# Optimization experiments

Measured on AMD Instinct MI355X. Metric: run time of the kernel, lower is better.

Reference implementation:

```python
import jax, jax.numpy as jnp
import numpy as np

# static config (matches init_kwargs)
C, NH, WS, H, W, NQ, PS = 384, 12, 8, 56, 56, 64, 8
HD = C // NH
SCALE = HD ** -0.5
EPS = 1e-5
MLP_H = 4 * C


def _rel_pos_index():
    ch, cw = np.meshgrid(np.arange(WS), np.arange(WS), indexing='ij')
    cf = np.stack([ch.ravel(), cw.ravel()])                      # [2, WS*WS]
    rel = cf[:, :, None] - cf[:, None, :]                        # [2, N, N]
    rel = rel.transpose(1, 2, 0)
    rel[:, :, 0] += WS - 1
    rel[:, :, 1] += WS - 1
    rel[:, :, 0] *= 2 * WS - 1
    return jnp.asarray(rel.sum(-1))                              # [N, N] int

REL_IDX = _rel_pos_index()


def _ln(x, g, b):
    mu = x.mean(-1, keepdims=True)
    var = ((x - mu) ** 2).mean(-1, keepdims=True)
    return (x - mu) * jax.lax.rsqrt(var + EPS) * g + b


def setup_inputs() -> dict:
    key = jax.random.key(0)
    ks = jax.random.split(key, 24)
    B = 16
    n = lambda k, shp, s=0.02: jax.random.normal(k, shp, dtype=jnp.float32) * s
    inp = {
        'x': jax.random.normal(ks[0], (B, H * W, C), dtype=jnp.float32),
        'query_tokens': n(ks[1], (1, NQ, C)),
        'kproj_w': n(ks[2], (C, C)), 'kproj_b': jnp.zeros((C,)),
        'kbn_g': jnp.ones((C,)), 'kbn_b': jnp.zeros((C,)),
        'vproj_w': n(ks[3], (C, C)), 'vproj_b': jnp.zeros((C,)),
        'vbn_g': jnp.ones((C,)), 'vbn_b': jnp.zeros((C,)),
        'ck_w': n(ks[4], (C, C)), 'ck_b': jnp.zeros((C,)),
        'cv_w': n(ks[5], (C, C)), 'cv_b': jnp.zeros((C,)),
        'qkv_w': n(ks[6], (C, 3 * C)), 'qkv_b': jnp.zeros((3 * C,)),
        'proj_w': n(ks[7], (C, C)), 'proj_b': jnp.zeros((C,)),
        'rpb_table': n(ks[8], ((2 * WS - 1) ** 2, NH)),
        'norm1_g': jnp.ones((C,)), 'norm1_b': jnp.zeros((C,)),
        'norm2_g': jnp.ones((C,)), 'norm2_b': jnp.zeros((C,)),
        'fc1_w': n(ks[9], (C, MLP_H)), 'fc1_b': jnp.zeros((MLP_H,)),
        'fc2_w': n(ks[10], (MLP_H, C)), 'fc2_b': jnp.zeros((C,)),
    }
    return inp


def _forward(x, query_tokens, kproj_w, kproj_b, kbn_g, kbn_b, vproj_w, vproj_b,
             vbn_g, vbn_b, ck_w, ck_b, cv_w, cv_b, qkv_w, qkv_b, proj_w, proj_b,
             rpb_table, norm1_g, norm1_b, norm2_g, norm2_b, fc1_w, fc1_b, fc2_w, fc2_b):
    B, L, _ = x.shape
    shortcut = x
    xn = _ln(x, norm1_g, norm1_b)                                # [B, L, C]

    # ---- global cross attention (pooled tokens -> learnable queries) ----
    x4 = xn.reshape(B, H, W, C)
    pooled = x4.reshape(B, H // PS, PS, W // PS, PS, C).mean(axis=(2, 4))  # [B,7,7,C]
    pooled = pooled.reshape(B, (H // PS) * (W // PS), C)         # [B, 49, C]
    # conv1x1 + BatchNorm2d (eval mode, default running stats mean=0, var=1)
    bn_scale = 1.0 / jnp.sqrt(1.0 + EPS)
    key = ((pooled @ kproj_w + kproj_b) * bn_scale) * kbn_g + kbn_b
    val = ((pooled @ vproj_w + vproj_b) * bn_scale) * vbn_g + vbn_b

    q = jnp.broadcast_to(query_tokens, (B, NQ, C))
    qh = q.reshape(B, NQ, NH, HD).transpose(0, 2, 1, 3)          # [B,NH,NQ,HD]
    kh = key.reshape(B, -1, NH, HD).transpose(0, 2, 1, 3)
    vh = val.reshape(B, -1, NH, HD).transpose(0, 2, 1, 3)
    attn = jax.nn.softmax(jnp.einsum('bhqd,bhkd->bhqk', qh, kh) * SCALE, axis=-1)
    o = jnp.einsum('bhqk,bhkd->bhqd', attn, vh).transpose(0, 2, 1, 3).reshape(B, NQ, C)
    gk = (o + q) @ ck_w + ck_b                                   # [B, NQ, C]
    gv = (o + q) @ cv_w + cv_b

    # ---- windowed attention with global kv concat ----
    nW = (H // WS) * (W // WS)
    N = WS * WS
    xw = (x4.reshape(B, H // WS, WS, W // WS, WS, C)
             .transpose(0, 1, 3, 2, 4, 5)
             .reshape(B * nW, N, C))                             # [B_, N, C]
    qkv = (xw @ qkv_w + qkv_b).reshape(B * nW, N, 3, NH, HD).transpose(2, 0, 3, 1, 4)
    wq, wk, wv = qkv[0], qkv[1], qkv[2]                          # [B_, NH, N, HD]

    gkh = jnp.broadcast_to(gk.reshape(B, 1, NQ, NH, HD), (B, nW, NQ, NH, HD))
    gkh = gkh.reshape(B * nW, NQ, NH, HD).transpose(0, 2, 1, 3)  # [B_, NH, NQ, HD]
    gvh = jnp.broadcast_to(gv.reshape(B, 1, NQ, NH, HD), (B, nW, NQ, NH, HD))
    gvh = gvh.reshape(B * nW, NQ, NH, HD).transpose(0, 2, 1, 3)
    wk = jnp.concatenate([wk, gkh], axis=2)                      # [B_, NH, N+NQ, HD]
    wv = jnp.concatenate([wv, gvh], axis=2)

    logits = jnp.einsum('bhqd,bhkd->bhqk', wq * SCALE, wk)       # [B_, NH, N, N+NQ]
    rpb = rpb_table[REL_IDX.reshape(-1)].reshape(N, N, NH).transpose(2, 0, 1)  # [NH,N,N]
    logits = logits.at[:, :, :, :N].add(rpb[None])
    wattn = jax.nn.softmax(logits, axis=-1)
    ow = jnp.einsum('bhqk,bhkd->bhqd', wattn, wv).transpose(0, 2, 1, 3).reshape(B * nW, N, C)
    ow = ow @ proj_w + proj_b

    # window reverse
    xr = (ow.reshape(B, H // WS, W // WS, WS, WS, C)
             .transpose(0, 1, 3, 2, 4, 5)
             .reshape(B, H * W, C))

    x = shortcut + xr
    h = jax.nn.gelu(_ln(x, norm2_g, norm2_b) @ fc1_w + fc1_b, approximate=False)
    return x + (h @ fc2_w + fc2_b)


def reference(x, query_tokens, kproj_w, kproj_b, kbn_g, kbn_b, vproj_w, vproj_b,
              vbn_g, vbn_b, ck_w, ck_b, cv_w, cv_b, qkv_w, qkv_b, proj_w, proj_b,
              rpb_table, norm1_g, norm1_b, norm2_g, norm2_b, fc1_w, fc1_b, fc2_w, fc2_b):
    return _forward(x, query_tokens, kproj_w, kproj_b, kbn_g, kbn_b, vproj_w, vproj_b,
                    vbn_g, vbn_b, ck_w, ck_b, cv_w, cv_b, qkv_w, qkv_b, proj_w, proj_b,
                    rpb_table, norm1_g, norm1_b, norm2_g, norm2_b, fc1_w, fc1_b, fc2_w, fc2_b)
```

## Files before the change

kernel.cpp:

```cpp
#include <hip/hip_runtime.h>
#include <math.h>

typedef __attribute__((ext_vector_type(8))) __bf16 bf16x8;
typedef __attribute__((ext_vector_type(4))) float f32x4;
typedef __attribute__((ext_vector_type(8))) unsigned short u16x8;

#define DI __device__ __forceinline__

DI float b2f(unsigned short u) { return __uint_as_float(((unsigned int)u) << 16); }
DI unsigned short f2b(float f) {
    unsigned int x = __float_as_uint(f);
    x += 0x7fffu + ((x >> 16) & 1u);
    return (unsigned short)(x >> 16);
}
DI unsigned short f2b_fast(float f) {
    __bf16 h = (__bf16)f;
    return *(unsigned short*)&h;
}

DI void gl16(const unsigned short* g, unsigned short* l) {
    __builtin_amdgcn_global_load_lds(
        (const __attribute__((address_space(1))) void*)g,
        (__attribute__((address_space(3))) void*)l,
        16, 0, 0);
}

DI float gelu_f(float v) {
    float y = -1.5957691216f * v - 0.0713548163f * v * v * v;
    return v * __builtin_amdgcn_rcpf(1.f + __expf(y));
}

#define SCALE_ATT 0.17677669529663687f
#define BN_SCALE  0.9999950000374997f

__global__ __launch_bounds__(256) void cvt_t_kernel(const float* __restrict__ in,
                                                    unsigned short* __restrict__ out,
                                                    int Kd, int Nd) {
    int i = blockIdx.x * 256 + threadIdx.x;
    if (i < Kd * Nd) {
        int k = i / Nd, n = i % Nd;
        out[(size_t)n * Kd + k] = f2b(in[i]);
    }
}

__global__ __launch_bounds__(64) void ln_kernel(const float* __restrict__ xin,
                                                const float* __restrict__ g,
                                                const float* __restrict__ bsh,
                                                unsigned short* __restrict__ out) {
    int row = blockIdx.x;
    int t = threadIdx.x;
    size_t base = (size_t)row * 384;
    float v[6];
    float s = 0.f;
#pragma unroll
    for (int p = 0; p < 6; ++p) { v[p] = xin[base + t + 64 * p]; s += v[p]; }
#pragma unroll
    for (int off = 32; off > 0; off >>= 1) s += __shfl_xor(s, off);
    float mu = s * (1.f / 384.f);
    float q = 0.f;
#pragma unroll
    for (int p = 0; p < 6; ++p) { float d = v[p] - mu; q += d * d; }
#pragma unroll
    for (int off = 32; off > 0; off >>= 1) q += __shfl_xor(q, off);
    float rstd = rsqrtf(q * (1.f / 384.f) + 1e-5f);
#pragma unroll
    for (int p = 0; p < 6; ++p) {
        int c = t + 64 * p;
        out[base + c] = f2b((v[p] - mu) * rstd * g[c] + bsh[c]);
    }
}

__global__ __launch_bounds__(384) void pool_kernel(const unsigned short* __restrict__ xn,
                                                   float* __restrict__ pooled) {
    int blk = blockIdx.x;
    int b = blk / 49, pp = blk % 49;
    int ph = pp / 7, pw = pp % 7;
    int c = threadIdx.x;
    float s = 0.f;
    for (int i = 0; i < 8; ++i) {
        size_t rb = ((size_t)b * 3136 + (size_t)(ph * 8 + i) * 56 + pw * 8) * 384;
        for (int j = 0; j < 8; ++j) s += b2f(xn[rb + (size_t)j * 384 + c]);
    }
    pooled[(size_t)blk * 384 + c] = s * (1.f / 64.f);
}

__global__ __launch_bounds__(128) void kvproj_kernel(
    const float* __restrict__ pooled,
    const float* __restrict__ kw, const float* __restrict__ kb,
    const float* __restrict__ kg, const float* __restrict__ kbb,
    const float* __restrict__ vw, const float* __restrict__ vb,
    const float* __restrict__ vg, const float* __restrict__ vbb,
    float* __restrict__ keyo, float* __restrict__ valo) {
    __shared__ float row[384];
    int r = blockIdx.x;
    int t = threadIdx.x;
    for (int c = t; c < 384; c += 128) row[c] = pooled[(size_t)r * 384 + c];
    __syncthreads();
#pragma unroll
    for (int p = 0; p < 3; ++p) {
        int c = t + 128 * p;
        float aK = 0.f, aV = 0.f;
        for (int k = 0; k < 384; ++k) {
            float rv = row[k];
            aK += rv * kw[(size_t)k * 384 + c];
            aV += rv * vw[(size_t)k * 384 + c];
        }
        keyo[(size_t)r * 384 + c] = (aK + kb[c]) * BN_SCALE * kg[c] + kbb[c];
        valo[(size_t)r * 384 + c] = (aV + vb[c]) * BN_SCALE * vg[c] + vbb[c];
    }
}

__global__ __launch_bounds__(64) void rpb_expand_kernel(const float* __restrict__ rpbt,
                                                        float* __restrict__ rpb_mat) {
    int h = blockIdx.x >> 6, q = blockIdx.x & 63;
    int k = threadIdx.x;
    int i1 = q >> 3, j1 = q & 7, i2 = k >> 3, j2 = k & 7;
    rpb_mat[((size_t)h * 64 + q) * 64 + k] = rpbt[(size_t)((i1 - i2 + 7) * 15 + (j1 - j2 + 7)) * 12 + h];
}

__global__ __launch_bounds__(64) void cross_attn_kernel(const float* __restrict__ keyg,
                                                        const float* __restrict__ valg,
                                                        const float* __restrict__ qtok,
                                                        float* __restrict__ o) {
    int b = blockIdx.x / 12, h = blockIdx.x % 12;
    __shared__ float kk[49][32];
    __shared__ float vv[49][32];
    int t = threadIdx.x;
    for (int idx = t; idx < 49 * 32; idx += 64) {
        int k = idx >> 5, d = idx & 31;
        size_t gidx = ((size_t)b * 49 + k) * 384 + h * 32 + d;
        kk[k][d] = keyg[gidx];
        vv[k][d] = valg[gidx];
    }
    __syncthreads();
    float q[32];
#pragma unroll
    for (int d = 0; d < 32; ++d) q[d] = qtok[(size_t)t * 384 + h * 32 + d] * SCALE_ATT;
    float lg[49];
    float mx = -1e30f;
#pragma unroll
    for (int k = 0; k < 49; ++k) {
        float s = 0.f;
#pragma unroll
        for (int d = 0; d < 32; ++d) s += q[d] * kk[k][d];
        lg[k] = s;
        mx = fmaxf(mx, s);
    }
    float sum = 0.f;
#pragma unroll
    for (int k = 0; k < 49; ++k) { float e = expf(lg[k] - mx); lg[k] = e; sum += e; }
    float inv = 1.f / sum;
    float od[32];
#pragma unroll
    for (int d = 0; d < 32; ++d) od[d] = 0.f;
#pragma unroll
    for (int k = 0; k < 49; ++k) {
        float wgt = lg[k];
#pragma unroll
        for (int d = 0; d < 32; ++d) od[d] += wgt * vv[k][d];
    }
#pragma unroll
    for (int d = 0; d < 32; ++d) o[((size_t)b * 64 + t) * 384 + h * 32 + d] = od[d] * inv;
}

__global__ __launch_bounds__(128) void gkv_kernel(
    const float* __restrict__ o, const float* __restrict__ qtok,
    const float* __restrict__ ckw, const float* __restrict__ ckb,
    const float* __restrict__ cvw, const float* __restrict__ cvb,
    unsigned short* __restrict__ gk, unsigned short* __restrict__ gv) {
    __shared__ float row[384];
    int r = blockIdx.x;
    int n = r & 63;
    int t = threadIdx.x;
    for (int c = t; c < 384; c += 128)
        row[c] = o[(size_t)r * 384 + c] + qtok[(size_t)n * 384 + c];
    __syncthreads();
#pragma unroll
    for (int p = 0; p < 3; ++p) {
        int c = t + 128 * p;
        float aK = 0.f, aV = 0.f;
        for (int k = 0; k < 384; ++k) {
            float rv = row[k];
            aK += rv * ckw[(size_t)k * 384 + c];
            aV += rv * cvw[(size_t)k * 384 + c];
        }
        gk[(size_t)r * 384 + c] = f2b(aK + ckb[c]);
        gv[(size_t)r * 384 + c] = f2b(aV + cvb[c]);
    }
}

template <int MODE>
__global__ __launch_bounds__(256, 3) void gemm128(const unsigned short* __restrict__ A,
                                                  const unsigned short* __restrict__ BT,
                                                  const float* __restrict__ bias,
                                                  int N, int K,
                                                  void* __restrict__ outp,
                                                  const void* __restrict__ aux0) {
    __shared__ __align__(16) unsigned short As[3][128 * 32];
    __shared__ __align__(16) unsigned short Bs[3][128 * 32];

    int nwg = gridDim.x * gridDim.y;
    int flat = blockIdx.y * gridDim.x + blockIdx.x;
    int flat2 = (flat & 7) * (nwg >> 3) + (flat >> 3);
    int bn = flat2 % gridDim.x, bm = flat2 / gridDim.x;

    int t = threadIdx.x;
    int w = t >> 6, lane = t & 63;
    int wm = w >> 1, wn = w & 1;
    int lo = lane & 15, g = lane >> 4;

    f32x4 acc[4][4];
#pragma unroll
    for (int i = 0; i < 4; ++i)
#pragma unroll
        for (int j = 0; j < 4; ++j) acc[i][j] = f32x4{0.f, 0.f, 0.f, 0.f};

    int srow = w * 32 + (lane >> 2);
    int schunk = (((lane & 3) ^ ((srow >> 1) & 3)) << 3);
    const unsigned short* Ap0 = A + (size_t)(bm * 128 + srow) * K + schunk;
    const unsigned short* Ap1 = A + (size_t)(bm * 128 + srow + 16) * K + schunk;
    const unsigned short* Bp0 = BT + (size_t)(bn * 128 + srow) * K + schunk;
    const unsigned short* Bp1 = BT + (size_t)(bn * 128 + srow + 16) * K + schunk;
    int d0 = (w * 32) * 32, d1 = (w * 32 + 16) * 32;

    int gx = ((g ^ ((lo >> 1) & 3)) << 3);

#define STAGE(buf, kb)                    \
    do {                                  \
        gl16(Ap0 + (kb), As[buf] + d0);   \
        gl16(Ap1 + (kb), As[buf] + d1);   \
        gl16(Bp0 + (kb), Bs[buf] + d0);   \
        gl16(Bp1 + (kb), Bs[buf] + d1);   \
    } while (0)

#define WAIT4() asm volatile("s_waitcnt vmcnt(4)" ::: "memory")
#define WAIT0() asm volatile("s_waitcnt vmcnt(0)" ::: "memory")

#define COMPUTE(buf)                                                                     \
    do {                                                                                 \
        bf16x8 af[4], bfv[4];                                                            \
        _Pragma("unroll")                                                                \
        for (int m = 0; m < 4; ++m)                                                      \
            af[m] = *(const bf16x8*)(As[buf] + (wm * 64 + m * 16 + lo) * 32 + gx);       \
        _Pragma("unroll")                                                                \
        for (int n = 0; n < 4; ++n)                                                      \
            bfv[n] = *(const bf16x8*)(Bs[buf] + (wn * 64 + n * 16 + lo) * 32 + gx);      \
        __builtin_amdgcn_s_setprio(1);                                                   \
        _Pragma("unroll")                                                                \
        for (int m = 0; m < 4; ++m)                                                      \
            _Pragma("unroll")                                                            \
            for (int n = 0; n < 4; ++n)                                                  \
                acc[m][n] = __builtin_amdgcn_mfma_f32_16x16x32_bf16(af[m], bfv[n],       \
                                                                    acc[m][n], 0, 0, 0); \
        __builtin_amdgcn_s_setprio(0);                                                   \
    } while (0)

    STAGE(0, 0);
    STAGE(1, 32);

    int nt = K >> 5;
    for (int tt = 0; tt < nt; tt += 3) {
        if (tt + 1 < nt) WAIT4(); else WAIT0();
        __builtin_amdgcn_s_barrier();
        if (tt + 2 < nt) STAGE(2, (tt + 2) * 32);
        COMPUTE(0);
        if (tt + 2 < nt) WAIT4(); else WAIT0();
        __builtin_amdgcn_s_barrier();
        if (tt + 3 < nt) STAGE(0, (tt + 3) * 32);
        COMPUTE(1);
        if (tt + 3 < nt) WAIT4(); else WAIT0();
        __builtin_amdgcn_s_barrier();
        if (tt + 4 < nt) STAGE(1, (tt + 4) * 32);
        COMPUTE(2);
    }
#undef STAGE
#undef WAIT4
#undef WAIT0
#undef COMPUTE

    int r0 = bm * 128 + wm * 64 + g * 4;
    int c0 = bn * 128 + wn * 64 + lo;
    int wgc = bm * 2 + wm;
    int bC = wgc / 49, winC = wgc % 49;
    int whC = winC / 7, wwC = winC % 7;
    int lC = (whC << 3) * 56 + (wwC << 3);
    size_t rowbaseC = (size_t)bC * 3136;
#pragma unroll
    for (int m = 0; m < 4; ++m)
#pragma unroll
        for (int n = 0; n < 4; ++n)
#pragma unroll
            for (int j = 0; j < 4; ++j) {
                int r = r0 + m * 16 + j;
                int c = c0 + n * 16;
                float v = acc[m][n][j] + bias[c];
                if (MODE == 0) {
                    ((unsigned short*)outp)[(size_t)r * N + c] = f2b(v);
                } else if (MODE == 1) {
                    int nn = m * 16 + (g << 2) + j;
                    int l = lC + (nn >> 3) * 56 + (nn & 7);
                    size_t idx = (rowbaseC + l) * 384 + c;
                    ((float*)outp)[idx] = ((const float*)aux0)[idx] + v;
                } else if (MODE == 2) {
                    ((unsigned short*)outp)[(size_t)r * N + c] = f2b(gelu_f(v));
                } else {
                    float res = ((const float*)aux0)[(size_t)r * 384 + c];
                    ((float*)outp)[(size_t)r * N + c] = v + res;
                }
            }
}

__global__ __launch_bounds__(64, 2) void win_attn_mfma(const unsigned short* __restrict__ qkv,
                                                       const unsigned short* __restrict__ gkb,
                                                       const unsigned short* __restrict__ gvb,
                                                       const float* __restrict__ rpb_mat,
                                                       unsigned short* __restrict__ ow) {
    int blk = blockIdx.x;
    int wg = blk / 12, h = blk % 12;
    int b = wg / 49, win = wg % 49;
    int wh = win / 7, ww = win % 7;
    int lane = threadIdx.x;
    int lo = lane & 15, g = lane >> 4;

    __shared__ __align__(16) unsigned short VT[32 * 136];
    __shared__ __align__(16) unsigned short PL[64 * 40];

    size_t qkvbase = (size_t)b * 3136 * 1152;
    int lbase = ((wh << 3)) * 56 + (ww << 3);

    {
        int n = lane;
        int l = lbase + (n >> 3) * 56 + (n & 7);
        const unsigned short* vp = qkv + qkvbase + (size_t)l * 1152 + 768 + h * 32;
        u16x8 v0 = *(const u16x8*)(vp);
        u16x8 v1 = *(const u16x8*)(vp + 8);
        u16x8 v2 = *(const u16x8*)(vp + 16);
        u16x8 v3 = *(const u16x8*)(vp + 24);
#pragma unroll
        for (int j = 0; j < 8; ++j) {
            VT[(0 + j) * 136 + n]  = v0[j];
            VT[(8 + j) * 136 + n]  = v1[j];
            VT[(16 + j) * 136 + n] = v2[j];
            VT[(24 + j) * 136 + n] = v3[j];
        }
        const unsigned short* gp = gvb + ((size_t)b * 64 + n) * 384 + h * 32;
        v0 = *(const u16x8*)(gp);
        v1 = *(const u16x8*)(gp + 8);
        v2 = *(const u16x8*)(gp + 16);
        v3 = *(const u16x8*)(gp + 24);
#pragma unroll
        for (int j = 0; j < 8; ++j) {
            VT[(0 + j) * 136 + 64 + n]  = v0[j];
            VT[(8 + j) * 136 + 64 + n]  = v1[j];
            VT[(16 + j) * 136 + 64 + n] = v2[j];
            VT[(24 + j) * 136 + 64 + n] = v3[j];
        }
    }

    bf16x8 qf[4];
#pragma unroll
    for (int qt = 0; qt < 4; ++qt) {
        int n = qt * 16 + lo;
        int l = lbase + (n >> 3) * 56 + (n & 7);
        qf[qt] = *(const bf16x8*)(qkv + qkvbase + (size_t)l * 1152 + h * 32 + g * 8);
    }

    f32x4 S[4][8];
#pragma unroll
    for (int qt = 0; qt < 4; ++qt)
#pragma unroll
        for (int t = 0; t < 8; ++t) S[qt][t] = f32x4{0.f, 0.f, 0.f, 0.f};

#pragma unroll
    for (int t = 0; t < 8; ++t) {
        bf16x8 kf;
        if (t < 4) {
            int key = t * 16 + lo;
            int l = lbase + (key >> 3) * 56 + (key & 7);
            kf = *(const bf16x8*)(qkv + qkvbase + (size_t)l * 1152 + 384 + h * 32 + g * 8);
        } else {
            int gkey = (t - 4) * 16 + lo;
            kf = *(const bf16x8*)(gkb + ((size_t)b * 64 + gkey) * 384 + h * 32 + g * 8);
        }
#pragma unroll
        for (int qt = 0; qt < 4; ++qt)
            S[qt][t] = __builtin_amdgcn_mfma_f32_16x16x32_bf16(qf[qt], kf, S[qt][t], 0, 0, 0);
    }

    const float* rb_h = rpb_mat + (size_t)h * 4096;
    float mx[4][4];
#pragma unroll
    for (int qt = 0; qt < 4; ++qt)
#pragma unroll
        for (int j = 0; j < 4; ++j) mx[qt][j] = -1e30f;

#pragma unroll
    for (int qt = 0; qt < 4; ++qt) {
#pragma unroll
        for (int t = 0; t < 8; ++t) {
#pragma unroll
            for (int j = 0; j < 4; ++j) {
                float v = S[qt][t][j] * SCALE_ATT;
                if (t < 4) v += rb_h[(qt * 16 + g * 4 + j) * 64 + t * 16 + lo];
                S[qt][t][j] = v;
                mx[qt][j] = fmaxf(mx[qt][j], v);
            }
        }
    }
#pragma unroll
    for (int qt = 0; qt < 4; ++qt)
#pragma unroll
        for (int j = 0; j < 4; ++j) {
#pragma unroll
            for (int m = 1; m <= 8; m <<= 1)
                mx[qt][j] = fmaxf(mx[qt][j], __shfl_xor(mx[qt][j], m));
        }

    float sm[4][4];
#pragma unroll
    for (int qt = 0; qt < 4; ++qt)
#pragma unroll
        for (int j = 0; j < 4; ++j) sm[qt][j] = 0.f;
#pragma unroll
    for (int qt = 0; qt < 4; ++qt)
#pragma unroll
        for (int t = 0; t < 8; ++t)
#pragma unroll
            for (int j = 0; j < 4; ++j) {
                float p = __expf(S[qt][t][j] - mx[qt][j]);
                S[qt][t][j] = p;
                sm[qt][j] += p;
            }
#pragma unroll
    for (int qt = 0; qt < 4; ++qt)
#pragma unroll
        for (int j = 0; j < 4; ++j) {
#pragma unroll
            for (int m = 1; m <= 8; m <<= 1)
                sm[qt][j] += __shfl_xor(sm[qt][j], m);
        }
    float inv[4][4];
#pragma unroll
    for (int qt = 0; qt < 4; ++qt)
#pragma unroll
        for (int j = 0; j < 4; ++j) inv[qt][j] = 1.f / sm[qt][j];

    f32x4 O[4][2];
#pragma unroll
    for (int qt = 0; qt < 4; ++qt)
#pragma unroll
        for (int dt = 0; dt < 2; ++dt) O[qt][dt] = f32x4{0.f, 0.f, 0.f, 0.f};

#pragma unroll
    for (int c = 0; c < 4; ++c) {
        __syncthreads();
#pragma unroll
        for (int qt = 0; qt < 4; ++qt) {
            int qb = qt * 16 + g * 4;
#pragma unroll
            for (int half = 0; half < 2; ++half) {
                int t = 2 * c + half;
#pragma unroll
                for (int j = 0; j < 4; ++j)
                    PL[(qb + j) * 40 + half * 16 + lo] = f2b_fast(S[qt][t][j]);
            }
        }
        __syncthreads();
#pragma unroll
        for (int qt = 0; qt < 4; ++qt) {
            bf16x8 pa = *(const bf16x8*)(PL + (qt * 16 + lo) * 40 + g * 8);
#pragma unroll
            for (int dt = 0; dt < 2; ++dt) {
                bf16x8 vb = *(const bf16x8*)(VT + (dt * 16 + lo) * 136 + c * 32 + g * 8);
                O[qt][dt] = __builtin_amdgcn_mfma_f32_16x16x32_bf16(pa, vb, O[qt][dt], 0, 0, 0);
            }
        }
    }

#pragma unroll
    for (int qt = 0; qt < 4; ++qt)
#pragma unroll
        for (int dt = 0; dt < 2; ++dt)
#pragma unroll
            for (int j = 0; j < 4; ++j) {
                int q = qt * 16 + g * 4 + j;
                int d = dt * 16 + lo;
                ow[((size_t)wg * 64 + q) * 384 + h * 32 + d] = f2b_fast(O[qt][dt][j] * inv[qt][j]);
            }
}

static const size_t OFF_XN   = 0;
static const size_t OFF_QKV  = 38535168;
static const size_t OFF_OW   = 154140672;
static const size_t OFF_X2   = 192675840;
static const size_t OFF_PL   = 269746176;
static const size_t OFF_KEY  = 270950400;
static const size_t OFF_VAL  = 272154624;
static const size_t OFF_O    = 273358848;
static const size_t OFF_GK   = 274931712;
static const size_t OFF_GV   = 276504576;
static const size_t OFF_QKVW = 278077440;
static const size_t OFF_PRJW = 278962176;
static const size_t OFF_FC1W = 279257088;
static const size_t OFF_FC2W = 280436736;

extern "C" void kernel_launch(void* const* d_in, const int* in_sizes, int n_in,
                              void* d_out, int out_size, void* d_ws, size_t ws_size,
                              hipStream_t stream) {
    const float* x      = (const float*)d_in[0];
    const float* qtok   = (const float*)d_in[1];
    const float* kprojw = (const float*)d_in[2];
    const float* kprojb = (const float*)d_in[3];
    const float* kbng   = (const float*)d_in[4];
    const float* kbnb   = (const float*)d_in[5];
    const float* vprojw = (const float*)d_in[6];
    const float* vprojb = (const float*)d_in[7];
    const float* vbng   = (const float*)d_in[8];
    const float* vbnb   = (const float*)d_in[9];
    const float* ckw    = (const float*)d_in[10];
    const float* ckb    = (const float*)d_in[11];
    const float* cvw    = (const float*)d_in[12];
    const float* cvb    = (const float*)d_in[13];
    const float* qkvw   = (const float*)d_in[14];
    const float* qkvb   = (const float*)d_in[15];
    const float* projw  = (const float*)d_in[16];
    const float* projb  = (const float*)d_in[17];
    const float* rpbt   = (const float*)d_in[18];
    const float* n1g    = (const float*)d_in[19];
    const float* n1b    = (const float*)d_in[20];
    const float* n2g    = (const float*)d_in[21];
    const float* n2b    = (const float*)d_in[22];
    const float* fc1w   = (const float*)d_in[23];
    const float* fc1b   = (const float*)d_in[24];
    const float* fc2w   = (const float*)d_in[25];
    const float* fc2b   = (const float*)d_in[26];

    char* wsb = (char*)d_ws;
    unsigned short* xn     = (unsigned short*)(wsb + OFF_XN);
    unsigned short* qkvbf  = (unsigned short*)(wsb + OFF_QKV);
    unsigned short* owbf   = (unsigned short*)(wsb + OFF_OW);
    float* x2      = (float*)(wsb + OFF_X2);
    float* pooled  = (float*)(wsb + OFF_PL);
    float* rpb_mat = (float*)(wsb + OFF_PL);
    float* keyg    = (float*)(wsb + OFF_KEY);
    float* valg    = (float*)(wsb + OFF_VAL);
    float* obuf    = (float*)(wsb + OFF_O);
    unsigned short* gkb = (unsigned short*)(wsb + OFF_GK);
    unsigned short* gvb = (unsigned short*)(wsb + OFF_GV);
    unsigned short* qkvw_t = (unsigned short*)(wsb + OFF_QKVW);
    unsigned short* prjw_t = (unsigned short*)(wsb + OFF_PRJW);
    unsigned short* fc1w_t = (unsigned short*)(wsb + OFF_FC1W);
    unsigned short* fc2w_t = (unsigned short*)(wsb + OFF_FC2W);
    unsigned short* ln2out = (unsigned short*)(wsb + OFF_XN);
    unsigned short* hbuf   = (unsigned short*)(wsb + OFF_QKV);

    cvt_t_kernel<<<(442368 + 255) / 256, 256, 0, stream>>>(qkvw, qkvw_t, 384, 1152);
    cvt_t_kernel<<<(147456 + 255) / 256, 256, 0, stream>>>(projw, prjw_t, 384, 384);
    cvt_t_kernel<<<(589824 + 255) / 256, 256, 0, stream>>>(fc1w, fc1w_t, 384, 1536);
    cvt_t_kernel<<<(589824 + 255) / 256, 256, 0, stream>>>(fc2w, fc2w_t, 1536, 384);
    ln_kernel<<<50176, 64, 0, stream>>>(x, n1g, n1b, xn);
    pool_kernel<<<784, 384, 0, stream>>>(xn, pooled);
    kvproj_kernel<<<784, 128, 0, stream>>>(pooled, kprojw, kprojb, kbng, kbnb,
                                           vprojw, vprojb, vbng, vbnb, keyg, valg);
    rpb_expand_kernel<<<768, 64, 0, stream>>>(rpbt, rpb_mat);
    cross_attn_kernel<<<192, 64, 0, stream>>>(keyg, valg, qtok, obuf);
    gkv_kernel<<<1024, 128, 0, stream>>>(obuf, qtok, ckw, ckb, cvw, cvb, gkb, gvb);
    gemm128<0><<<dim3(9, 392), 256, 0, stream>>>(xn, qkvw_t, qkvb, 1152, 384, qkvbf, nullptr);
    win_attn_mfma<<<9408, 64, 0, stream>>>(qkvbf, gkb, gvb, rpb_mat, owbf);
    gemm128<1><<<dim3(3, 392), 256, 0, stream>>>(owbf, prjw_t, projb, 384, 384, x2, x);
    ln_kernel<<<50176, 64, 0, stream>>>(x2, n2g, n2b, ln2out);
    gemm128<2><<<dim3(12, 392), 256, 0, stream>>>(ln2out, fc1w_t, fc1b, 1536, 384, hbuf, nullptr);
    gemm128<3><<<dim3(3, 392), 256, 0, stream>>>(hbuf, fc2w_t, fc2b, 384, 1536, (float*)d_out, x2);
}
```

Baseline: 696.8 us.

## Load GEMM B operand directly to registers, fuse weight conversions, single-pass LayerNorm

The GEMM now reads the B (weight) fragments from global memory straight into a triple-buffered register array instead of staging them through LDS. This halves shared-memory use and drops the LDS reads for B, at the cost of more VGPRs and uncoalesced per-lane global loads. The four weight transpose-convert launches are merged into one kernel. LayerNorm switches to float2 loads, packed bf16 stores, and a one-pass E[x^2]-mu^2 variance, which is slightly less numerically robust.

```diff
diff --git a/kernel.cpp b/kernel.cpp
--- a/kernel.cpp
+++ b/kernel.cpp
@@ -33,10 +33,19 @@
 #define SCALE_ATT 0.17677669529663687f
 #define BN_SCALE  0.9999950000374997f
 
-__global__ __launch_bounds__(256) void cvt_t_kernel(const float* __restrict__ in,
-                                                    unsigned short* __restrict__ out,
-                                                    int Kd, int Nd) {
-    int i = blockIdx.x * 256 + threadIdx.x;
+__global__ __launch_bounds__(256) void cvt_all(const float* __restrict__ s0, const float* __restrict__ s1,
+                                               const float* __restrict__ s2, const float* __restrict__ s3,
+                                               unsigned short* __restrict__ d0, unsigned short* __restrict__ d1,
+                                               unsigned short* __restrict__ d2, unsigned short* __restrict__ d3) {
+    int b = blockIdx.x;
+    const float* in;
+    unsigned short* out;
+    int Kd, Nd, i0;
+    if (b < 1728)      { in = s0; out = d0; Kd = 384;  Nd = 1152; i0 = b * 256; }
+    else if (b < 2304) { in = s1; out = d1; Kd = 384;  Nd = 384;  i0 = (b - 1728) * 256; }
+    else if (b < 4608) { in = s2; out = d2; Kd = 384;  Nd = 1536; i0 = (b - 2304) * 256; }
+    else               { in = s3; out = d3; Kd = 1536; Nd = 384;  i0 = (b - 4608) * 256; }
+    int i = i0 + threadIdx.x;
     if (i < Kd * Nd) {
         int k = i / Nd, n = i % Nd;
         out[(size_t)n * Kd + k] = f2b(in[i]);
@@ -50,23 +59,27 @@
     int row = blockIdx.x;
     int t = threadIdx.x;
     size_t base = (size_t)row * 384;
-    float v[6];
-    float s = 0.f;
-#pragma unroll
-    for (int p = 0; p < 6; ++p) { v[p] = xin[base + t + 64 * p]; s += v[p]; }
-#pragma unroll
-    for (int off = 32; off > 0; off >>= 1) s += __shfl_xor(s, off);
+    float2 v[3];
+    float s = 0.f, q = 0.f;
+#pragma unroll
+    for (int p = 0; p < 3; ++p) {
+        v[p] = *(const float2*)(xin + base + p * 128 + t * 2);
+        s += v[p].x + v[p].y;
+        q += v[p].x * v[p].x + v[p].y * v[p].y;
+    }
+#pragma unroll
+    for (int off = 32; off > 0; off >>= 1) {
+        s += __shfl_xor(s, off);
+        q += __shfl_xor(q, off);
+    }
     float mu = s * (1.f / 384.f);
-    float q = 0.f;
-#pragma unroll
-    for (int p = 0; p < 6; ++p) { float d = v[p] - mu; q += d * d; }
-#pragma unroll
-    for (int off = 32; off > 0; off >>= 1) q += __shfl_xor(q, off);
-    float rstd = rsqrtf(q * (1.f / 384.f) + 1e-5f);
-#pragma unroll
-    for (int p = 0; p < 6; ++p) {
-        int c = t + 64 * p;
-        out[base + c] = f2b((v[p] - mu) * rstd * g[c] + bsh[c]);
+    float rstd = rsqrtf(q * (1.f / 384.f) - mu * mu + 1e-5f);
+#pragma unroll
+    for (int p = 0; p < 3; ++p) {
+        int c = p * 128 + t * 2;
+        unsigned int lo16 = f2b((v[p].x - mu) * rstd * g[c] + bsh[c]);
+        unsigned int hi16 = f2b((v[p].y - mu) * rstd * g[c + 1] + bsh[c + 1]);
+        ((unsigned int*)(out + base + p * 128))[t] = lo16 | (hi16 << 16);
     }
 }
 
@@ -197,7 +210,6 @@
                                                   void* __restrict__ outp,
                                                   const void* __restrict__ aux0) {
     __shared__ __align__(16) unsigned short As[3][128 * 32];
-    __shared__ __align__(16) unsigned short Bs[3][128 * 32];
 
     int nwg = gridDim.x * gridDim.y;
     int flat = blockIdx.y * gridDim.x + blockIdx.x;
@@ -219,62 +231,68 @@
     int schunk = (((lane & 3) ^ ((srow >> 1) & 3)) << 3);
     const unsigned short* Ap0 = A + (size_t)(bm * 128 + srow) * K + schunk;
     const unsigned short* Ap1 = A + (size_t)(bm * 128 + srow + 16) * K + schunk;
-    const unsigned short* Bp0 = BT + (size_t)(bn * 128 + srow) * K + schunk;
-    const unsigned short* Bp1 = BT + (size_t)(bn * 128 + srow + 16) * K + schunk;
     int d0 = (w * 32) * 32, d1 = (w * 32 + 16) * 32;
-
     int gx = ((g ^ ((lo >> 1) & 3)) << 3);
+
+    const unsigned short* Bbase = BT + (size_t)(bn * 128 + wn * 64 + lo) * K + g * 8;
+    size_t nK16 = (size_t)16 * K;
+    bf16x8 Breg[3][4];
 
 #define STAGE(buf, kb)                    \
     do {                                  \
         gl16(Ap0 + (kb), As[buf] + d0);   \
         gl16(Ap1 + (kb), As[buf] + d1);   \
-        gl16(Bp0 + (kb), Bs[buf] + d0);   \
-        gl16(Bp1 + (kb), Bs[buf] + d1);   \
     } while (0)
 
-#define WAIT4() asm volatile("s_waitcnt vmcnt(4)" ::: "memory")
+#define LOADB(slot, kb)                                                        \
+    do {                                                                       \
+        _Pragma("unroll")                                                      \
+        for (int n = 0; n < 4; ++n)                                            \
+            Breg[slot][n] = *(const bf16x8*)(Bbase + (size_t)n * nK16 + (kb)); \
+    } while (0)
+
+#define WAIT6() asm volatile("s_waitcnt vmcnt(6)" ::: "memory")
 #define WAIT0() asm volatile("s_waitcnt vmcnt(0)" ::: "memory")
 
-#define COMPUTE(buf)                                                                     \
+#define COMPUTE(slot)                                                                    \
     do {                                                                                 \
-        bf16x8 af[4], bfv[4];                                                            \
+        bf16x8 af[4];                                                                    \
         _Pragma("unroll")                                                                \
         for (int m = 0; m < 4; ++m)                                                      \
-            af[m] = *(const bf16x8*)(As[buf] + (wm * 64 + m * 16 + lo) * 32 + gx);       \
-        _Pragma("unroll")                                                                \
-        for (int n = 0; n < 4; ++n)                                                      \
-            bfv[n] = *(const bf16x8*)(Bs[buf] + (wn * 64 + n * 16 + lo) * 32 + gx);      \
+            af[m] = *(const bf16x8*)(As[slot] + (wm * 64 + m * 16 + lo) * 32 + gx);      \
         __builtin_amdgcn_s_setprio(1);                                                   \
         _Pragma("unroll")                                                                \
         for (int m = 0; m < 4; ++m)                                                      \
             _Pragma("unroll")                                                            \
             for (int n = 0; n < 4; ++n)                                                  \
-                acc[m][n] = __builtin_amdgcn_mfma_f32_16x16x32_bf16(af[m], bfv[n],       \
+                acc[m][n] = __builtin_amdgcn_mfma_f32_16x16x32_bf16(af[m], Breg[slot][n],\
                                                                     acc[m][n], 0, 0, 0); \
         __builtin_amdgcn_s_setprio(0);                                                   \
     } while (0)
 
     STAGE(0, 0);
+    LOADB(0, 0);
     STAGE(1, 32);
+    LOADB(1, 32);
 
     int nt = K >> 5;
     for (int tt = 0; tt < nt; tt += 3) {
-        if (tt + 1 < nt) WAIT4(); else WAIT0();
+        if (tt + 1 < nt) WAIT6(); else WAIT0();
         __builtin_amdgcn_s_barrier();
-        if (tt + 2 < nt) STAGE(2, (tt + 2) * 32);
+        if (tt + 2 < nt) { STAGE(2, (tt + 2) * 32); LOADB(2, (tt + 2) * 32); }
         COMPUTE(0);
-        if (tt + 2 < nt) WAIT4(); else WAIT0();
+        if (tt + 2 < nt) WAIT6(); else WAIT0();
         __builtin_amdgcn_s_barrier();
-        if (tt + 3 < nt) STAGE(0, (tt + 3) * 32);
+        if (tt + 3 < nt) { STAGE(0, (tt + 3) * 32); LOADB(0, (tt + 3) * 32); }
         COMPUTE(1);
-        if (tt + 3 < nt) WAIT4(); else WAIT0();
+        if (tt + 3 < nt) WAIT6(); else WAIT0();
         __builtin_amdgcn_s_barrier();
-        if (tt + 4 < nt) STAGE(1, (tt + 4) * 32);
+        if (tt + 4 < nt) { STAGE(1, (tt + 4) * 32); LOADB(1, (tt + 4) * 32); }
         COMPUTE(2);
     }
 #undef STAGE
-#undef WAIT4
+#undef LOADB
+#undef WAIT6
 #undef WAIT0
 #undef COMPUTE
 
@@ -554,10 +572,7 @@
     unsigned short* ln2out = (unsigned short*)(wsb + OFF_XN);
     unsigned short* hbuf   = (unsigned short*)(wsb + OFF_QKV);
 
-    cvt_t_kernel<<<(442368 + 255) / 256, 256, 0, stream>>>(qkvw, qkvw_t, 384, 1152);
-    cvt_t_kernel<<<(147456 + 255) / 256, 256, 0, stream>>>(projw, prjw_t, 384, 384);
-    cvt_t_kernel<<<(589824 + 255) / 256, 256, 0, stream>>>(fc1w, fc1w_t, 384, 1536);
-    cvt_t_kernel<<<(589824 + 255) / 256, 256, 0, stream>>>(fc2w, fc2w_t, 1536, 384);
+    cvt_all<<<6912, 256, 0, stream>>>(qkvw, projw, fc1w, fc2w, qkvw_t, prjw_t, fc1w_t, fc2w_t);
     ln_kernel<<<50176, 64, 0, stream>>>(x, n1g, n1b, xn);
     pool_kernel<<<784, 384, 0, stream>>>(xn, pooled);
     kvproj_kernel<<<784, 128, 0, stream>>>(pooled, kprojw, kprojb, kbng, kbnb,
```

Result: slower. 812.1 us (+16.6%).
